# Performance work log

Measured on AMD Instinct MI355X. Metric: run time of the kernel, lower is better.

Reference implementation:

```python
import jax, jax.numpy as jnp
import numpy as np

B, Q, M, H, D = 2, 2048, 2048, 16, 64
HID = H * D           # hidden_size == num_heads * head_size
K_LEN = M + Q         # key/value length after memory concat
EPS = 1e-3            # keras LayerNormalization default epsilon
RAMP = 32             # Adaptive_Span ramp_size
NEG = -1e9


def setup_inputs() -> dict:
    key = jax.random.key(0)
    ks = jax.random.split(key, 12)
    s = 0.02
    return {
        "query": jax.random.normal(ks[0], (B, Q, HID), jnp.float32),
        "memory": jax.random.normal(ks[1], (B, M, HID), jnp.float32),
        "Wq": jax.random.normal(ks[2], (HID, H * D), jnp.float32) * s,
        "Wk": jax.random.normal(ks[3], (HID, H * D), jnp.float32) * s,
        "Wv": jax.random.normal(ks[4], (HID, H * D), jnp.float32) * s,
        "Wo": jax.random.normal(ks[5], (H * D, HID), jnp.float32) * s,
        "Wr": jax.random.normal(ks[6], (HID, H * D), jnp.float32) * s,
        "gamma_mem": jnp.ones((HID,), jnp.float32),
        "beta_mem": jnp.zeros((HID,), jnp.float32),
        "gamma_q": jnp.ones((HID,), jnp.float32),
        "beta_q": jnp.zeros((HID,), jnp.float32),
        "r_w_bias": jax.random.normal(ks[7], (1, H, 1, D), jnp.float32) * s,
        "r_r_bias": jax.random.normal(ks[8], (1, H, 1, D), jnp.float32) * s,
        "span_val": jnp.zeros((1, H, 1, 1), jnp.float32),
    }


def _layer_norm(x, gamma, beta):
    mu = jnp.mean(x, axis=-1, keepdims=True)
    var = jnp.mean(jnp.square(x - mu), axis=-1, keepdims=True)
    return (x - mu) * jax.lax.rsqrt(var + EPS) * gamma + beta


def _rel_shift(x):
    # Transformer-XL relative shift on [B,H,Q,K]
    b, h, q, k = x.shape
    x = jnp.pad(x, ((0, 0), (0, 0), (0, 0), (1, 0)))
    x = x.reshape(b, h, k + 1, q)[:, :, 1:, :]
    return x.reshape(b, h, q, k)


def reference(query, memory, Wq, Wk, Wv, Wo, Wr,
              gamma_mem, beta_mem, gamma_q, beta_q,
              r_w_bias, r_r_bias, span_val):
    kv = jnp.concatenate([memory, query], axis=1)          # [B,K,HID]
    kv = _layer_norm(kv, gamma_mem, beta_mem)
    q_in = _layer_norm(query, gamma_q, beta_q)

    # sinusoidal relative position embedding, positions K-1 .. 0
    pos_seq = jnp.arange(K_LEN - 1, -1, -1, dtype=jnp.float32)
    inv_freq = 1.0 / (10000.0 ** (jnp.arange(0, HID, 2, dtype=jnp.float32) / HID))
    sin_inp = pos_seq[:, None] * inv_freq[None, :]
    pos_emb = jnp.concatenate([jnp.sin(sin_inp), jnp.cos(sin_inp)], axis=-1)  # [K,HID]

    q = (q_in @ Wq).reshape(B, Q, H, D).transpose(0, 2, 1, 3)      # [B,H,Q,D]
    k = (kv @ Wk).reshape(B, K_LEN, H, D).transpose(0, 2, 1, 3)    # [B,H,K,D]
    v = (kv @ Wv).reshape(B, K_LEN, H, D).transpose(0, 2, 1, 3)    # [B,H,K,D]
    rel = (pos_emb @ Wr).reshape(K_LEN, H, D).transpose(1, 0, 2)   # [H,K,D]

    AD = jnp.einsum('bhqd,bhkd->bhqk', q + r_w_bias, k)
    BD = _rel_shift(jnp.einsum('bhqd,hkd->bhqk', q + r_r_bias, rel))
    logits = (AD + BD) / D                                          # note: /head_size, not sqrt

    # causal bias over the query block, zeros over memory columns
    causal = jnp.triu(jnp.ones((Q, Q), jnp.float32), 1) * NEG
    bias = jnp.concatenate([jnp.zeros((Q, M), jnp.float32), causal], axis=-1)
    logits = logits + bias[None, None]

    w = jax.nn.softmax(logits, axis=-1)                             # [B,H,Q,K]

    # adaptive span masking (static current_val path)
    mt = jnp.arange(Q, dtype=jnp.float32)
    span_mask = jnp.clip((mt[None, None, None, :] + span_val * Q) / (RAMP + 1), 0.0, 1.0)
    full_mask = jnp.concatenate(
        [jnp.ones((1, H, 1, M), jnp.float32),
         jnp.broadcast_to(span_mask, (1, H, 1, Q))], axis=-1)       # [1,H,1,K]
    w = w * full_mask
    w = w / (jnp.sum(w, axis=-1, keepdims=True) + 1e-8)

    out = jnp.einsum('bhqk,bhkd->bhqd', w, v)
    out = out.transpose(0, 2, 1, 3).reshape(B, Q, H * D)
    return out @ Wo
```

## Files before the change

kernel.cpp:

```cpp
#include <hip/hip_runtime.h>
#include <hip/hip_bf16.h>
#include <math.h>

#define B_   2
#define Q_   2048
#define M_   2048
#define H_   16
#define D_   64
#define HID_ 1024
#define KL_  4096
#define RT_  128
#define WT_  64
#define LSCL 0.022542110013890053f

typedef short short8 __attribute__((ext_vector_type(8)));
typedef short short4v __attribute__((ext_vector_type(4)));
typedef float f32x4 __attribute__((ext_vector_type(4)));
typedef float f32x16 __attribute__((ext_vector_type(16)));
typedef unsigned int uint2v __attribute__((ext_vector_type(2)));

__device__ __forceinline__ void async_copy16(const void* g, void* l) {
  __builtin_amdgcn_global_load_lds((const __attribute__((address_space(1))) unsigned int*)g,
                                   (__attribute__((address_space(3))) unsigned int*)l,
                                   16, 0, 0);
}

__device__ __forceinline__ float ldin(const void* p, size_t i, int md) {
  return md ? ((const float*)p)[i] : __bfloat162float(((const __hip_bfloat16*)p)[i]);
}

__device__ __forceinline__ short bfbits(float v) {
  __hip_bfloat16 t = __float2bfloat16(v);
  return *(short*)&t;
}

__device__ __forceinline__ float fexp2(float x) { return exp2f(x); }

__global__ __launch_bounds__(256) void detect_kernel(const unsigned int* __restrict__ q,
                                                     int* __restrict__ flag) {
  __shared__ int cnt;
  if (threadIdx.x == 0) cnt = 0;
  __syncthreads();
  int ins = 0;
#pragma unroll
  for (int i = 0; i < 4; i++) {
    unsigned int u = q[threadIdx.x * 4 + i];
    int e0 = (int)((u >> 7) & 0xffu);
    int e1 = (int)((u >> 23) & 0xffu);
    if (e0 == 0xff || e0 < 102 || e0 > 140) ins++;
    if (e1 == 0xff || e1 < 102 || e1 > 140) ins++;
  }
  atomicAdd(&cnt, ins);
  __syncthreads();
  if (threadIdx.x == 0) *flag = (cnt > 512) ? 1 : 0;
}

__global__ __launch_bounds__(256) void wtpe_kernel(
    const void* __restrict__ s0, const void* __restrict__ s1, const void* __restrict__ s2,
    const void* __restrict__ s3, const void* __restrict__ s4,
    __hip_bfloat16* __restrict__ d0, __hip_bfloat16* __restrict__ d1,
    __hip_bfloat16* __restrict__ d2, __hip_bfloat16* __restrict__ d3,
    __hip_bfloat16* __restrict__ d4, __hip_bfloat16* __restrict__ pe,
    const int* __restrict__ mode) {
  const int tid = threadIdx.x;
  if (blockIdx.z >= 5) {
    const int p = (blockIdx.z - 5) * 256 + blockIdx.y * 16 + blockIdx.x;
    const float pos = (float)(KL_ - 1 - p);
#pragma unroll
    for (int i = 0; i < 4; i++) {
      int c = tid * 4 + i;
      int f = (c < 512) ? c : c - 512;
      float invf = fexp2(-(float)f * (13.287712379549449f / 512.0f));
      float a = pos * invf;
      float v = (c < 512) ? __sinf(a) : __cosf(a);
      pe[(size_t)p * HID_ + c] = __float2bfloat16(v);
    }
    return;
  }
  const int md = *mode;
  const void* src; __hip_bfloat16* dst;
  switch (blockIdx.z) {
    case 0: src = s0; dst = d0; break;
    case 1: src = s1; dst = d1; break;
    case 2: src = s2; dst = d2; break;
    case 3: src = s3; dst = d3; break;
    default: src = s4; dst = d4; break;
  }
  const int r0 = blockIdx.x * 64, c0 = blockIdx.y * 64;
  __shared__ __hip_bfloat16 t[64][65];
  const int col = tid & 63, r4 = tid >> 6;
#pragma unroll
  for (int i = 0; i < 16; i++)
    t[r4 + i * 4][col] = __float2bfloat16(ldin(src, (size_t)(r0 + r4 + i * 4) * HID_ + c0 + col, md));
  __syncthreads();
#pragma unroll
  for (int i = 0; i < 16; i++)
    dst[(size_t)(c0 + r4 + i * 4) * HID_ + r0 + col] = t[col][r4 + i * 4];
}

__global__ __launch_bounds__(256) void ln_kernel(
    const void* __restrict__ mem, const void* __restrict__ qry,
    const void* __restrict__ gmem, const void* __restrict__ bmem,
    const void* __restrict__ gq, const void* __restrict__ bq,
    __hip_bfloat16* __restrict__ kvout, __hip_bfloat16* __restrict__ qout,
    const int* __restrict__ mode) {
  const int md = *mode;
  const int row = blockIdx.x;
  const void* src;
  const void* gamma; const void* beta;
  size_t base;
  __hip_bfloat16* dst;
  if (row < B_ * KL_) {
    const int b = row / KL_, j = row % KL_;
    if (j < M_) { src = mem; base = ((size_t)b * M_ + j) * HID_; }
    else        { src = qry; base = ((size_t)b * Q_ + (j - M_)) * HID_; }
    gamma = gmem; beta = bmem;
    dst = kvout + (size_t)row * HID_;
  } else {
    const int r = row - B_ * KL_;
    src = qry; base = (size_t)r * HID_;
    gamma = gq; beta = bq;
    dst = qout + (size_t)r * HID_;
  }
  const int tid = threadIdx.x;
  float x[4];
  float s = 0.f, ss = 0.f;
#pragma unroll
  for (int i = 0; i < 4; i++) {
    x[i] = ldin(src, base + i * 256 + tid, md);
    s += x[i]; ss += x[i] * x[i];
  }
#pragma unroll
  for (int o = 32; o > 0; o >>= 1) { s += __shfl_down(s, o); ss += __shfl_down(ss, o); }
  __shared__ float red[8];
  if ((tid & 63) == 0) { red[(tid >> 6) * 2] = s; red[(tid >> 6) * 2 + 1] = ss; }
  __syncthreads();
  float ts = 0.f, tss = 0.f;
#pragma unroll
  for (int i = 0; i < 4; i++) { ts += red[i * 2]; tss += red[i * 2 + 1]; }
  const float mu = ts * (1.f / 1024.f);
  const float var = tss * (1.f / 1024.f) - mu * mu;
  const float rs = rsqrtf(var + 1e-3f);
#pragma unroll
  for (int i = 0; i < 4; i++) {
    int c = i * 256 + tid;
    dst[c] = __float2bfloat16((x[i] - mu) * rs * ldin(gamma, c, md) + ldin(beta, c, md));
  }
}

template <int WRITE_MODE_SWITCH>
__device__ __forceinline__ void gemm_body(const __hip_bfloat16* __restrict__ A,
                                          const __hip_bfloat16* __restrict__ BT,
                                          void* __restrict__ C, int md, float scl) {
  __shared__ __attribute__((aligned(16))) __hip_bfloat16 sA[128 * 32];
  __shared__ __attribute__((aligned(16))) __hip_bfloat16 sB[128 * 32];
  const int tid = threadIdx.x;
  const int lane = tid & 63;
  const int w = tid >> 6;
  const int quad = lane >> 4, l16 = lane & 15;
  const int m0 = blockIdx.x * 128;
  const int n0 = blockIdx.y * 128;
  const int wm = (w >> 1) * 64, wn = (w & 1) * 64;
  const f32x4 fz = {0.f, 0.f, 0.f, 0.f};

  f32x4 acc[4][4];
#pragma unroll
  for (int i = 0; i < 4; i++)
#pragma unroll
    for (int j = 0; j < 4; j++) acc[i][j] = fz;

  for (int kk = 0; kk < HID_ / 32; kk++) {
    const int k0 = kk * 32;
    __syncthreads();
#pragma unroll
    for (int t = 0; t < 2; t++) {
      int c = (w * 2 + t) * 64 + lane;
      int row = c >> 2;
      int cid = (c & 3) ^ (row & 3);
      async_copy16(A + (size_t)(m0 + row) * HID_ + k0 + cid * 8, (char*)sA + c * 16);
      async_copy16(BT + (size_t)(n0 + row) * HID_ + k0 + cid * 8, (char*)sB + c * 16);
    }
    __syncthreads();
    short8 af[4], bf[4];
#pragma unroll
    for (int mt = 0; mt < 4; mt++) {
      int r = wm + mt * 16 + l16;
      af[mt] = *(const short8*)((const char*)sA + r * 64 + ((quad ^ (r & 3)) * 16));
    }
#pragma unroll
    for (int nt = 0; nt < 4; nt++) {
      int r = wn + nt * 16 + l16;
      bf[nt] = *(const short8*)((const char*)sB + r * 64 + ((quad ^ (r & 3)) * 16));
    }
#pragma unroll
    for (int mt = 0; mt < 4; mt++)
#pragma unroll
      for (int nt = 0; nt < 4; nt++)
        acc[mt][nt] = __builtin_amdgcn_mfma_f32_16x16x32_bf16(af[mt], bf[nt], acc[mt][nt], 0, 0, 0);
  }
#pragma unroll
  for (int mt = 0; mt < 4; mt++)
#pragma unroll
    for (int nt = 0; nt < 4; nt++)
#pragma unroll
      for (int rg = 0; rg < 4; rg++) {
        int r = m0 + wm + mt * 16 + quad * 4 + rg;
        int cc = n0 + wn + nt * 16 + l16;
        size_t idx = (size_t)r * HID_ + cc;
        if (WRITE_MODE_SWITCH && md) ((float*)C)[idx] = acc[mt][nt][rg];
        else ((__hip_bfloat16*)C)[idx] = __float2bfloat16(acc[mt][nt][rg] * scl);
      }
}

__global__ __launch_bounds__(256) void gemm_bt128(const __hip_bfloat16* __restrict__ A,
                                                  const __hip_bfloat16* __restrict__ BT,
                                                  __hip_bfloat16* __restrict__ C, float scl) {
  gemm_body<0>(A, BT, (void*)C, 0, scl);
}

__global__ __launch_bounds__(256) void gemm_out(const __hip_bfloat16* __restrict__ A,
                                                const __hip_bfloat16* __restrict__ BT,
                                                void* __restrict__ C,
                                                const int* __restrict__ mode) {
  gemm_body<1>(A, BT, C, *mode, 1.0f);
}

__global__ __launch_bounds__(256) void gemm_q(const __hip_bfloat16* __restrict__ A,
                                              const __hip_bfloat16* __restrict__ BT,
                                              const void* __restrict__ rwb,
                                              const void* __restrict__ rrb,
                                              __hip_bfloat16* __restrict__ qw,
                                              __hip_bfloat16* __restrict__ qr,
                                              const int* __restrict__ mode) {
  const int md = *mode;
  __shared__ __attribute__((aligned(16))) __hip_bfloat16 sA[128 * 32];
  __shared__ __attribute__((aligned(16))) __hip_bfloat16 sB[128 * 32];
  const int tid = threadIdx.x;
  const int lane = tid & 63;
  const int w = tid >> 6;
  const int quad = lane >> 4, l16 = lane & 15;
  const int m0 = blockIdx.x * 128;
  const int n0 = blockIdx.y * 128;
  const int wm = (w >> 1) * 64, wn = (w & 1) * 64;
  const f32x4 fz = {0.f, 0.f, 0.f, 0.f};

  f32x4 acc[4][4];
#pragma unroll
  for (int i = 0; i < 4; i++)
#pragma unroll
    for (int j = 0; j < 4; j++) acc[i][j] = fz;

  for (int kk = 0; kk < HID_ / 32; kk++) {
    const int k0 = kk * 32;
    __syncthreads();
#pragma unroll
    for (int t = 0; t < 2; t++) {
      int c = (w * 2 + t) * 64 + lane;
      int row = c >> 2;
      int cid = (c & 3) ^ (row & 3);
      async_copy16(A + (size_t)(m0 + row) * HID_ + k0 + cid * 8, (char*)sA + c * 16);
      async_copy16(BT + (size_t)(n0 + row) * HID_ + k0 + cid * 8, (char*)sB + c * 16);
    }
    __syncthreads();
    short8 af[4], bf[4];
#pragma unroll
    for (int mt = 0; mt < 4; mt++) {
      int r = wm + mt * 16 + l16;
      af[mt] = *(const short8*)((const char*)sA + r * 64 + ((quad ^ (r & 3)) * 16));
    }
#pragma unroll
    for (int nt = 0; nt < 4; nt++) {
      int r = wn + nt * 16 + l16;
      bf[nt] = *(const short8*)((const char*)sB + r * 64 + ((quad ^ (r & 3)) * 16));
    }
#pragma unroll
    for (int mt = 0; mt < 4; mt++)
#pragma unroll
      for (int nt = 0; nt < 4; nt++)
        acc[mt][nt] = __builtin_amdgcn_mfma_f32_16x16x32_bf16(af[mt], bf[nt], acc[mt][nt], 0, 0, 0);
  }
  float bw[4], br[4];
#pragma unroll
  for (int nt = 0; nt < 4; nt++) {
    int cc = n0 + wn + nt * 16 + l16;
    bw[nt] = ldin(rwb, cc, md);
    br[nt] = ldin(rrb, cc, md);
  }
#pragma unroll
  for (int mt = 0; mt < 4; mt++)
#pragma unroll
    for (int nt = 0; nt < 4; nt++)
#pragma unroll
      for (int rg = 0; rg < 4; rg++) {
        int r = m0 + wm + mt * 16 + quad * 4 + rg;
        int cc = n0 + wn + nt * 16 + l16;
        size_t idx = (size_t)r * HID_ + cc;
        float a = acc[mt][nt][rg];
        qw[idx] = __float2bfloat16((a + bw[nt]) * LSCL);
        qr[idx] = __float2bfloat16((a + br[nt]) * LSCL);
      }
}

__global__ __launch_bounds__(256) void gemm_dualv(const __hip_bfloat16* __restrict__ A,
                                                  const __hip_bfloat16* __restrict__ BT,
                                                  __hip_bfloat16* __restrict__ C0,
                                                  __hip_bfloat16* __restrict__ vpt) {
  __shared__ __attribute__((aligned(16))) __hip_bfloat16 sA[128 * 32];
  __shared__ __attribute__((aligned(16))) __hip_bfloat16 sB[128 * 32];
  __shared__ __attribute__((aligned(16))) short sT[128 * 136];
  const int tid = threadIdx.x;
  const int lane = tid & 63;
  const int w = tid >> 6;
  const int quad = lane >> 4, l16 = lane & 15;
  const int m0 = blockIdx.x * 128;
  const int n0 = blockIdx.y * 128;
  const int wm = (w >> 1) * 64, wn = (w & 1) * 64;
  const f32x4 fz = {0.f, 0.f, 0.f, 0.f};

  f32x4 acc[4][4];
#pragma unroll
  for (int i = 0; i < 4; i++)
#pragma unroll
    for (int j = 0; j < 4; j++) acc[i][j] = fz;

  for (int kk = 0; kk < HID_ / 32; kk++) {
    const int k0 = kk * 32;
    __syncthreads();
#pragma unroll
    for (int t = 0; t < 2; t++) {
      int c = (w * 2 + t) * 64 + lane;
      int row = c >> 2;
      int cid = (c & 3) ^ (row & 3);
      async_copy16(A + (size_t)(m0 + row) * HID_ + k0 + cid * 8, (char*)sA + c * 16);
      async_copy16(BT + (size_t)(n0 + row) * HID_ + k0 + cid * 8, (char*)sB + c * 16);
    }
    __syncthreads();
    short8 af[4], bf[4];
#pragma unroll
    for (int mt = 0; mt < 4; mt++) {
      int r = wm + mt * 16 + l16;
      af[mt] = *(const short8*)((const char*)sA + r * 64 + ((quad ^ (r & 3)) * 16));
    }
#pragma unroll
    for (int nt = 0; nt < 4; nt++) {
      int r = wn + nt * 16 + l16;
      bf[nt] = *(const short8*)((const char*)sB + r * 64 + ((quad ^ (r & 3)) * 16));
    }
#pragma unroll
    for (int mt = 0; mt < 4; mt++)
#pragma unroll
      for (int nt = 0; nt < 4; nt++)
        acc[mt][nt] = __builtin_amdgcn_mfma_f32_16x16x32_bf16(af[mt], bf[nt], acc[mt][nt], 0, 0, 0);
  }
  if (n0 < HID_) {
#pragma unroll
    for (int mt = 0; mt < 4; mt++)
#pragma unroll
      for (int nt = 0; nt < 4; nt++)
#pragma unroll
        for (int rg = 0; rg < 4; rg++) {
          int r = m0 + wm + mt * 16 + quad * 4 + rg;
          int cc = n0 + wn + nt * 16 + l16;
          C0[(size_t)r * HID_ + cc] = __float2bfloat16(acc[mt][nt][rg]);
        }
  } else {
#pragma unroll
    for (int mt = 0; mt < 4; mt++)
#pragma unroll
      for (int nt = 0; nt < 4; nt++) {
        int r = wm + mt * 16 + quad * 4;
        int cc = wn + nt * 16 + l16;
        short4v pk;
#pragma unroll
        for (int rg = 0; rg < 4; rg++) pk[rg] = bfbits(acc[mt][nt][rg]);
        *(short4v*)&sT[cc * 136 + r] = pk;
      }
    __syncthreads();
    const int b = m0 >> 12;
    const int j0g = m0 & (KL_ - 1);
    const int cg0 = n0 - HID_;
#pragma unroll
    for (int it = 0; it < 16; it++) {
      int cc = it * 8 + w * 2 + (lane >> 5);
      int jj = (lane & 31) * 4;
      int cg = cg0 + cc;
      int h = cg >> 6, d = cg & 63;
      short4v v = *(const short4v*)&sT[cc * 136 + jj];
      *(short4v*)(vpt + (((size_t)(b * H_ + h)) * D_ + d) * KL_ + j0g + jj) = v;
    }
  }
}

__global__ __launch_bounds__(256, 2) void attn_kernel(
    const __hip_bfloat16* __restrict__ qpw, const __hip_bfloat16* __restrict__ qpr,
    const __hip_bfloat16* __restrict__ kp, const __hip_bfloat16* __restrict__ vpt,
    const __hip_bfloat16* __restrict__ relp,
    const void* __restrict__ spanv, __hip_bfloat16* __restrict__ attn_out,
    const int* __restrict__ mode) {
  const int md = *mode;
  const int bid = blockIdx.x;
  int rk = (bid >> 3) & 15;
  if (bid & 256) rk ^= 15;
  const int i0 = rk << 7;
  const int bh = (bid & 7) + 8 * (bid >> 7);
  const int b = bh >> 4, h = bh & 15;

  const int tid = threadIdx.x;
  const int lane = tid & 63;
  const int w = tid >> 6;
  const int l31 = lane & 31, hi = lane >> 5;
  const int di = w * 32 + l31;
  const int iRow = i0 + di;

  __shared__ __attribute__((aligned(16))) __hip_bfloat16 sk[64 * 64];
  __shared__ __attribute__((aligned(16))) __hip_bfloat16 srel[192 * 64];
  __shared__ __attribute__((aligned(16))) __hip_bfloat16 svt[64 * 64];
  __shared__ __attribute__((aligned(16))) short sTP[128 * 100];

  const int rb = di * 200;
  const int sw = l31 & 7;

  const __hip_bfloat16* kbase = kp + (size_t)b * KL_ * HID_ + h * D_;
  const __hip_bfloat16* vtb = vpt + ((size_t)(b * H_ + h)) * D_ * KL_;
  const float sv = ldin(spanv, h, md);
  const float svQ = sv * (float)Q_;
  const int pb0 = Q_ - RT_ - i0;
  const int wof = (3 - w) * 32;
  const int ntiles = ((M_ + i0 + RT_ - 1) >> 6) + 1;

  const f32x16 z16 = {0.f,0.f,0.f,0.f,0.f,0.f,0.f,0.f,0.f,0.f,0.f,0.f,0.f,0.f,0.f,0.f};

  short8 qf[4], qrf[4];
  {
    const size_t qofs = ((size_t)(b * Q_ + iRow)) * HID_ + h * D_;
#pragma unroll
    for (int ks = 0; ks < 4; ks++) {
      qf[ks]  = *(const short8*)(qpw + qofs + ks * 16 + hi * 8);
      qrf[ks] = *(const short8*)(qpr + qofs + ks * 16 + hi * 8);
    }
  }

  {
#pragma unroll
    for (int t = 0; t < 2; t++) {
      int c = (w * 2 + t) * 64 + lane;
      int row = c >> 3;
      int cid = (c & 7) ^ (row & 7);
      async_copy16(kbase + (size_t)row * HID_ + cid * 8, (char*)sk + c * 16);
      async_copy16(vtb + (size_t)row * KL_ + cid * 8, (char*)svt + c * 16);
    }
#pragma unroll
    for (int t = 0; t < 6; t++) {
      int c = (w * 6 + t) * 64 + lane;
      int row = c >> 3;
      int cid = (c & 7) ^ (row & 7);
      int p = pb0 + row; p = p < KL_ ? p : KL_ - 1;
      async_copy16(relp + (size_t)p * HID_ + h * D_ + cid * 8, (char*)srel + c * 16);
    }
  }

  float mrow = -3e38f, lrow = 0.f, dfrow = 0.f;
  f32x16 oacc[2];
  oacc[0] = z16; oacc[1] = z16;
  int rot = 0;

  for (int kt = 0; kt < ntiles; kt++) {
    const int j0 = kt * WT_;

    __syncthreads();

    short8 rK[2], rR[2], rV[2];
    const bool pf = (kt + 1 < ntiles);
    {
      int j0n = j0 + WT_; if (j0n > KL_ - WT_) j0n = KL_ - WT_;
#pragma unroll
      for (int t = 0; t < 2; t++) {
        int c = (w * 2 + t) * 64 + lane;
        int row = c >> 3;
        int cid = (c & 7) ^ (row & 7);
        rK[t] = *(const short8*)(kbase + (size_t)(j0n + row) * HID_ + cid * 8);
        rV[t] = *(const short8*)(vtb + (size_t)row * KL_ + j0n + cid * 8);
        int p = pb0 + (kt + 1) * 64 + 128 + row; p = p < KL_ ? p : KL_ - 1;
        rR[t] = *(const short8*)(relp + (size_t)p * HID_ + h * D_ + cid * 8);
      }
    }
    __builtin_amdgcn_sched_barrier(0);

    __builtin_amdgcn_s_setprio(1);
    f32x16 S[2];
    S[0] = z16; S[1] = z16;
#pragma unroll
    for (int mt = 0; mt < 2; mt++) {
      const char* rowp = (const char*)sk + (mt * 32 + l31) * 128;
#pragma unroll
      for (int ks = 0; ks < 4; ks++) {
        short8 af = *(const short8*)(rowp + (((ks * 2 + hi) ^ sw) * 16));
        S[mt] = __builtin_amdgcn_mfma_f32_32x32x16_bf16(af, qf[ks], S[mt], 0, 0, 0);
      }
    }

#pragma unroll
    for (int mt = 0; mt < 3; mt++) {
      f32x16 T = z16;
      int rr = wof + mt * 32 + l31 + rot; if (rr >= 192) rr -= 192;
      const char* rowp = (const char*)srel + rr * 128;
#pragma unroll
      for (int ks = 0; ks < 4; ks++) {
        short8 af = *(const short8*)(rowp + (((ks * 2 + hi) ^ sw) * 16));
        T = __builtin_amdgcn_mfma_f32_32x32x16_bf16(af, qrf[ks], T, 0, 0, 0);
      }
#pragma unroll
      for (int r2 = 0; r2 < 4; r2++) {
        short4v pk;
#pragma unroll
        for (int r4 = 0; r4 < 4; r4++) pk[r4] = bfbits(T[r2 * 4 + r4]);
        *(short4v*)((char*)sTP + rb + (mt * 32 + 8 * r2 + 4 * hi) * 2) = pk;
      }
    }
    __builtin_amdgcn_s_setprio(0);

    {
      const char* tb2 = (const char*)sTP + rb + (31 - l31 + 4 * hi) * 2;
#pragma unroll
      for (int mt = 0; mt < 2; mt++)
#pragma unroll
        for (int r2 = 0; r2 < 4; r2++)
#pragma unroll
          for (int r4 = 0; r4 < 4; r4++)
            S[mt][r2 * 4 + r4] +=
                __bfloat162float(*(const __hip_bfloat16*)(tb2 + (mt * 32 + 8 * r2 + r4) * 2));
    }

    const bool causalT = (j0 + WT_ - 1 - i0) > M_;
    float mnew = mrow;
#pragma unroll
    for (int mt = 0; mt < 2; mt++)
#pragma unroll
      for (int r2 = 0; r2 < 4; r2++)
#pragma unroll
        for (int r4 = 0; r4 < 4; r4++) {
          float v = S[mt][r2 * 4 + r4];
          if (causalT) {
            int j = j0 + mt * 32 + 8 * r2 + 4 * hi + r4;
            if (j - iRow > M_) v = -1e30f;
          }
          S[mt][r2 * 4 + r4] = v;
          mnew = fmaxf(mnew, v);
        }
    mnew = fmaxf(mnew, __shfl_xor(mnew, 32));
    if (!__all(mnew - mrow <= 8.f)) {
      const float alpha = fexp2(mrow - mnew);
      mrow = mnew;
      lrow *= alpha; dfrow *= alpha;
#pragma unroll
      for (int dt = 0; dt < 2; dt++)
#pragma unroll
        for (int rg = 0; rg < 16; rg++) oacc[dt][rg] *= alpha;
    }

    const bool maskT = (j0 + WT_ > M_) && ((float)j0 < (float)M_ + 33.f - svQ);
    short8 paf[4];
#pragma unroll
    for (int mt = 0; mt < 2; mt++) {
      unsigned Pp[4][2];
#pragma unroll
      for (int r2 = 0; r2 < 4; r2++) {
        short4v g;
#pragma unroll
        for (int r4 = 0; r4 < 4; r4++) {
          float pv = fexp2(S[mt][r2 * 4 + r4] - mrow);
          lrow += pv;
          float pm = pv;
          if (maskT) {
            int j = j0 + mt * 32 + 8 * r2 + 4 * hi + r4;
            if (j >= M_) {
              float t0 = (float)(j - M_) + svQ;
              float mk = fminf(fmaxf(t0 * (1.0f / 33.0f), 0.f), 1.f);
              pm = pv * mk;
              dfrow += pv - pm;
            }
          }
          g[r4] = bfbits(pm);
        }
        union { short4v s; unsigned u[2]; } cv; cv.s = g;
        Pp[r2][0] = cv.u[0]; Pp[r2][1] = cv.u[1];
      }
#pragma unroll
      for (int half = 0; half < 2; half++) {
        uint2v rA = __builtin_amdgcn_permlane32_swap(Pp[half * 2][0], Pp[half * 2 + 1][0], false, false);
        uint2v rB = __builtin_amdgcn_permlane32_swap(Pp[half * 2][1], Pp[half * 2 + 1][1], false, false);
        union { unsigned u[4]; short8 s; } asm8;
        asm8.u[0] = rA[0]; asm8.u[1] = rB[0]; asm8.u[2] = rA[1]; asm8.u[3] = rB[1];
        paf[mt * 2 + half] = asm8.s;
      }
    }

    __builtin_amdgcn_s_setprio(1);
#pragma unroll
    for (int dt = 0; dt < 2; dt++) {
      const char* rowp = (const char*)svt + (dt * 32 + l31) * 128;
#pragma unroll
      for (int ks = 0; ks < 4; ks++) {
        short8 bfv = *(const short8*)(rowp + (((ks * 2 + hi) ^ sw) * 16));
        oacc[dt] = __builtin_amdgcn_mfma_f32_32x32x16_bf16(bfv, paf[ks], oacc[dt], 0, 0, 0);
      }
    }
    __builtin_amdgcn_s_setprio(0);

    __syncthreads();

    if (pf) {
#pragma unroll
      for (int t = 0; t < 2; t++) {
        int c = (w * 2 + t) * 64 + lane;
        int row = c >> 3;
        *(short8*)((char*)sk + c * 16) = rK[t];
        *(short8*)((char*)svt + c * 16) = rV[t];
        *(short8*)((char*)srel + (rot + row) * 128 + (c & 7) * 16) = rR[t];
      }
    }
    rot += 64; if (rot == 192) rot = 0;
  }

  lrow += __shfl_xor(lrow, 32);
  dfrow += __shfl_xor(dfrow, 32);
  const float denom = (lrow - dfrow) + 1e-8f * lrow;
  const float rdenom = 1.f / denom;
  __hip_bfloat16* ob = attn_out + ((size_t)(b * Q_ + iRow)) * HID_ + h * D_;
#pragma unroll
  for (int dt = 0; dt < 2; dt++)
#pragma unroll
    for (int r2 = 0; r2 < 4; r2++) {
      short4v o;
#pragma unroll
      for (int r4 = 0; r4 < 4; r4++) o[r4] = bfbits(oacc[dt][r2 * 4 + r4] * rdenom);
      *(short4v*)(ob + dt * 32 + 8 * r2 + 4 * hi) = o;
    }
}

extern "C" void kernel_launch(void* const* d_in, const int* in_sizes, int n_in,
                              void* d_out, int out_size, void* d_ws, size_t ws_size,
                              hipStream_t stream) {
  const void* query  = d_in[0];
  const void* memory = d_in[1];
  const void* Wq = d_in[2];
  const void* Wk = d_in[3];
  const void* Wv = d_in[4];
  const void* Wo = d_in[5];
  const void* Wr = d_in[6];
  const void* gmem = d_in[7];
  const void* bmem = d_in[8];
  const void* gq = d_in[9];
  const void* bq = d_in[10];
  const void* rwb = d_in[11];
  const void* rrb = d_in[12];
  const void* spanv = d_in[13];

  char* ws = (char*)d_ws;
  size_t off = 0;
  auto alloc = [&](size_t bytes) -> char* {
    char* p = ws + off;
    off += (bytes + 255) & ~(size_t)255;
    return p;
  };
  int* flag = (int*)alloc(256);
  const size_t SZ_W = (size_t)HID_ * HID_ * 2;
  __hip_bfloat16* wqT = (__hip_bfloat16*)alloc(SZ_W);
  __hip_bfloat16* wkT = (__hip_bfloat16*)alloc(SZ_W);
  __hip_bfloat16* wvT = (__hip_bfloat16*)alloc(SZ_W);
  __hip_bfloat16* wrT = (__hip_bfloat16*)alloc(SZ_W);
  __hip_bfloat16* woT = (__hip_bfloat16*)alloc(SZ_W);
  __hip_bfloat16* kvln = (__hip_bfloat16*)alloc((size_t)B_ * KL_ * HID_ * 2);
  __hip_bfloat16* qln  = (__hip_bfloat16*)alloc((size_t)B_ * Q_ * HID_ * 2);
  __hip_bfloat16* pe   = (__hip_bfloat16*)alloc((size_t)KL_ * HID_ * 2);
  __hip_bfloat16* qpw  = (__hip_bfloat16*)alloc((size_t)B_ * Q_ * HID_ * 2);
  __hip_bfloat16* qpr  = (__hip_bfloat16*)alloc((size_t)B_ * Q_ * HID_ * 2);
  __hip_bfloat16* kpb  = (__hip_bfloat16*)alloc((size_t)B_ * KL_ * HID_ * 2);
  __hip_bfloat16* vptb = (__hip_bfloat16*)alloc((size_t)B_ * KL_ * HID_ * 2);
  __hip_bfloat16* relp = (__hip_bfloat16*)alloc((size_t)KL_ * HID_ * 2);
  __hip_bfloat16* aout = (__hip_bfloat16*)alloc((size_t)B_ * Q_ * HID_ * 2);

  dim3 tb(256);
  detect_kernel<<<dim3(1), tb, 0, stream>>>((const unsigned int*)query, flag);

  wtpe_kernel<<<dim3(16, 16, 21), tb, 0, stream>>>(Wq, Wk, Wv, Wr, Wo,
                                                   wqT, wkT, wvT, wrT, woT, pe, flag);

  ln_kernel<<<dim3(B_ * KL_ + B_ * Q_), tb, 0, stream>>>(memory, query, gmem, bmem, gq, bq,
                                                         kvln, qln, flag);

  gemm_q<<<dim3(B_ * Q_ / 128, HID_ / 128), tb, 0, stream>>>(qln, wqT, rwb, rrb, qpw, qpr, flag);
  gemm_dualv<<<dim3(B_ * KL_ / 128, 2 * HID_ / 128), tb, 0, stream>>>(kvln, wkT, kpb, vptb);
  gemm_bt128<<<dim3(KL_ / 128, HID_ / 128), tb, 0, stream>>>(pe, wrT, relp, 1.0f);

  attn_kernel<<<dim3((Q_ / RT_) * H_ * B_), tb, 0, stream>>>(qpw, qpr, kpb, vptb, relp, spanv, aout, flag);

  gemm_out<<<dim3(B_ * Q_ / 128, HID_ / 128), tb, 0, stream>>>(aout, woT, d_out, flag);

  (void)in_sizes; (void)n_in; (void)out_size; (void)ws_size;
}
```

Before: 497.0 us.

## Load V fragments directly to registers and double-buffer K/rel tiles to drop a barrier

V^T fragments for the PV MFMA are now loaded straight from global memory into registers, with a one-tile register prefetch (vA/vB), instead of being staged through shared memory. K tiles are double-buffered in LDS and the rel ring grows from 192 to 256 rows, so each iteration needs one __syncthreads instead of two. This is meant to cut LDS traffic and barrier stalls in the attention loop. The cost is 16 extra short8 registers per thread, which may lower occupancy, plus uncoalesced per-lane global V reads.

```diff
diff --git a/kernel.cpp b/kernel.cpp
--- a/kernel.cpp
+++ b/kernel.cpp
@@ -412,9 +412,8 @@
   const int di = w * 32 + l31;
   const int iRow = i0 + di;
 
-  __shared__ __attribute__((aligned(16))) __hip_bfloat16 sk[64 * 64];
-  __shared__ __attribute__((aligned(16))) __hip_bfloat16 srel[192 * 64];
-  __shared__ __attribute__((aligned(16))) __hip_bfloat16 svt[64 * 64];
+  __shared__ __attribute__((aligned(16))) __hip_bfloat16 sk[2 * 64 * 64];
+  __shared__ __attribute__((aligned(16))) __hip_bfloat16 srel[256 * 64];
   __shared__ __attribute__((aligned(16))) short sTP[128 * 100];
 
   const int rb = di * 200;
@@ -440,6 +439,13 @@
     }
   }
 
+  short8 vA[8], vB[8];
+#pragma unroll
+  for (int dt = 0; dt < 2; dt++)
+#pragma unroll
+    for (int ks = 0; ks < 4; ks++)
+      vA[dt * 4 + ks] = *(const short8*)(vtb + (size_t)(dt * 32 + l31) * KL_ + ks * 16 + hi * 8);
+
   {
 #pragma unroll
     for (int t = 0; t < 2; t++) {
@@ -447,7 +453,6 @@
       int row = c >> 3;
       int cid = (c & 7) ^ (row & 7);
       async_copy16(kbase + (size_t)row * HID_ + cid * 8, (char*)sk + c * 16);
-      async_copy16(vtb + (size_t)row * KL_ + cid * 8, (char*)svt + c * 16);
     }
 #pragma unroll
     for (int t = 0; t < 6; t++) {
@@ -464,25 +469,31 @@
   oacc[0] = z16; oacc[1] = z16;
   int rot = 0;
 
+  __syncthreads();
+
   for (int kt = 0; kt < ntiles; kt++) {
     const int j0 = kt * WT_;
-
-    __syncthreads();
-
-    short8 rK[2], rR[2], rV[2];
+    const char* skr = (const char*)sk + (kt & 1) * 8192;
+    char* skw = (char*)sk + ((kt + 1) & 1) * 8192;
     const bool pf = (kt + 1 < ntiles);
+    int j0n = j0 + WT_; if (j0n > KL_ - WT_) j0n = KL_ - WT_;
+
+    short8 rK[2], rR[2];
     {
-      int j0n = j0 + WT_; if (j0n > KL_ - WT_) j0n = KL_ - WT_;
 #pragma unroll
       for (int t = 0; t < 2; t++) {
         int c = (w * 2 + t) * 64 + lane;
         int row = c >> 3;
         int cid = (c & 7) ^ (row & 7);
         rK[t] = *(const short8*)(kbase + (size_t)(j0n + row) * HID_ + cid * 8);
-        rV[t] = *(const short8*)(vtb + (size_t)row * KL_ + j0n + cid * 8);
-        int p = pb0 + (kt + 1) * 64 + 128 + row; p = p < KL_ ? p : KL_ - 1;
+        int p = pb0 + kt * 64 + 192 + row; p = p < KL_ ? p : KL_ - 1;
         rR[t] = *(const short8*)(relp + (size_t)p * HID_ + h * D_ + cid * 8);
       }
+#pragma unroll
+      for (int dt = 0; dt < 2; dt++)
+#pragma unroll
+        for (int ks = 0; ks < 4; ks++)
+          vB[dt * 4 + ks] = *(const short8*)(vtb + (size_t)(dt * 32 + l31) * KL_ + j0n + ks * 16 + hi * 8);
     }
     __builtin_amdgcn_sched_barrier(0);
 
@@ -491,7 +502,7 @@
     S[0] = z16; S[1] = z16;
 #pragma unroll
     for (int mt = 0; mt < 2; mt++) {
-      const char* rowp = (const char*)sk + (mt * 32 + l31) * 128;
+      const char* rowp = skr + (mt * 32 + l31) * 128;
 #pragma unroll
       for (int ks = 0; ks < 4; ks++) {
         short8 af = *(const short8*)(rowp + (((ks * 2 + hi) ^ sw) * 16));
@@ -502,7 +513,7 @@
 #pragma unroll
     for (int mt = 0; mt < 3; mt++) {
       f32x16 T = z16;
-      int rr = wof + mt * 32 + l31 + rot; if (rr >= 192) rr -= 192;
+      int rr = (wof + mt * 32 + l31 + rot) & 255;
       const char* rowp = (const char*)srel + rr * 128;
 #pragma unroll
       for (int ks = 0; ks < 4; ks++) {
@@ -597,29 +608,27 @@
 
     __builtin_amdgcn_s_setprio(1);
 #pragma unroll
-    for (int dt = 0; dt < 2; dt++) {
-      const char* rowp = (const char*)svt + (dt * 32 + l31) * 128;
-#pragma unroll
-      for (int ks = 0; ks < 4; ks++) {
-        short8 bfv = *(const short8*)(rowp + (((ks * 2 + hi) ^ sw) * 16));
-        oacc[dt] = __builtin_amdgcn_mfma_f32_32x32x16_bf16(bfv, paf[ks], oacc[dt], 0, 0, 0);
-      }
-    }
+    for (int dt = 0; dt < 2; dt++)
+#pragma unroll
+      for (int ks = 0; ks < 4; ks++)
+        oacc[dt] = __builtin_amdgcn_mfma_f32_32x32x16_bf16(vA[dt * 4 + ks], paf[ks], oacc[dt], 0, 0, 0);
     __builtin_amdgcn_s_setprio(0);
-
-    __syncthreads();
 
     if (pf) {
 #pragma unroll
       for (int t = 0; t < 2; t++) {
         int c = (w * 2 + t) * 64 + lane;
         int row = c >> 3;
-        *(short8*)((char*)sk + c * 16) = rK[t];
-        *(short8*)((char*)svt + c * 16) = rV[t];
-        *(short8*)((char*)srel + (rot + row) * 128 + (c & 7) * 16) = rR[t];
-      }
-    }
-    rot += 64; if (rot == 192) rot = 0;
+        *(short8*)(skw + c * 16) = rK[t];
+        int cr = (rot + 192 + row) & 255;
+        *(short8*)((char*)srel + cr * 128 + (c & 7) * 16) = rR[t];
+      }
+    }
+#pragma unroll
+    for (int i = 0; i < 8; i++) vA[i] = vB[i];
+    rot = (rot + 64) & 255;
+
+    __syncthreads();
   }
 
   lrow += __shfl_xor(lrow, 32);
```

Measured after the change: 514.0 us. 1.03x slower.

## Double GEMM K-tile to 64 and tree-reduce attention row max and sum

Applied to the files above, without the earlier changes.

The projection GEMMs now stage 64-wide K slices in LDS with an 8-way XOR swizzle, halving the number of barrier-separated load phases per tile. gemm_dualv aliases its transpose buffer onto the A/B staging area to keep LDS use flat, which needs an extra barrier before the transpose write. In the attention kernel, the causal mask is applied in a separate pass, and the row max and row sum are computed as shallow trees instead of serial chains to shorten dependency latency. The larger tiles raise LDS per block and may lower occupancy.

```diff
diff --git a/kernel.cpp b/kernel.cpp
--- a/kernel.cpp
+++ b/kernel.cpp
@@ -152,8 +152,8 @@
 __device__ __forceinline__ void gemm_body(const __hip_bfloat16* __restrict__ A,
                                           const __hip_bfloat16* __restrict__ BT,
                                           void* __restrict__ C, int md, float scl) {
-  __shared__ __attribute__((aligned(16))) __hip_bfloat16 sA[128 * 32];
-  __shared__ __attribute__((aligned(16))) __hip_bfloat16 sB[128 * 32];
+  __shared__ __attribute__((aligned(16))) __hip_bfloat16 sA[128 * 64];
+  __shared__ __attribute__((aligned(16))) __hip_bfloat16 sB[128 * 64];
   const int tid = threadIdx.x;
   const int lane = tid & 63;
   const int w = tid >> 6;
@@ -169,34 +169,37 @@
 #pragma unroll
     for (int j = 0; j < 4; j++) acc[i][j] = fz;
 
-  for (int kk = 0; kk < HID_ / 32; kk++) {
-    const int k0 = kk * 32;
-    __syncthreads();
-#pragma unroll
-    for (int t = 0; t < 2; t++) {
-      int c = (w * 2 + t) * 64 + lane;
-      int row = c >> 2;
-      int cid = (c & 3) ^ (row & 3);
+  for (int kk = 0; kk < HID_ / 64; kk++) {
+    const int k0 = kk * 64;
+    __syncthreads();
+#pragma unroll
+    for (int t = 0; t < 4; t++) {
+      int c = (w * 4 + t) * 64 + lane;
+      int row = c >> 3;
+      int cid = (c & 7) ^ (row & 7);
       async_copy16(A + (size_t)(m0 + row) * HID_ + k0 + cid * 8, (char*)sA + c * 16);
       async_copy16(BT + (size_t)(n0 + row) * HID_ + k0 + cid * 8, (char*)sB + c * 16);
     }
     __syncthreads();
-    short8 af[4], bf[4];
-#pragma unroll
-    for (int mt = 0; mt < 4; mt++) {
-      int r = wm + mt * 16 + l16;
-      af[mt] = *(const short8*)((const char*)sA + r * 64 + ((quad ^ (r & 3)) * 16));
-    }
-#pragma unroll
-    for (int nt = 0; nt < 4; nt++) {
-      int r = wn + nt * 16 + l16;
-      bf[nt] = *(const short8*)((const char*)sB + r * 64 + ((quad ^ (r & 3)) * 16));
-    }
-#pragma unroll
-    for (int mt = 0; mt < 4; mt++)
-#pragma unroll
-      for (int nt = 0; nt < 4; nt++)
-        acc[mt][nt] = __builtin_amdgcn_mfma_f32_16x16x32_bf16(af[mt], bf[nt], acc[mt][nt], 0, 0, 0);
+#pragma unroll
+    for (int half = 0; half < 2; half++) {
+      short8 af[4], bf[4];
+#pragma unroll
+      for (int mt = 0; mt < 4; mt++) {
+        int r = wm + mt * 16 + l16;
+        af[mt] = *(const short8*)((const char*)sA + r * 128 + (((half * 4 + quad) ^ (r & 7)) * 16));
+      }
+#pragma unroll
+      for (int nt = 0; nt < 4; nt++) {
+        int r = wn + nt * 16 + l16;
+        bf[nt] = *(const short8*)((const char*)sB + r * 128 + (((half * 4 + quad) ^ (r & 7)) * 16));
+      }
+#pragma unroll
+      for (int mt = 0; mt < 4; mt++)
+#pragma unroll
+        for (int nt = 0; nt < 4; nt++)
+          acc[mt][nt] = __builtin_amdgcn_mfma_f32_16x16x32_bf16(af[mt], bf[nt], acc[mt][nt], 0, 0, 0);
+    }
   }
 #pragma unroll
   for (int mt = 0; mt < 4; mt++)
@@ -233,8 +236,8 @@
                                               __hip_bfloat16* __restrict__ qr,
                                               const int* __restrict__ mode) {
   const int md = *mode;
-  __shared__ __attribute__((aligned(16))) __hip_bfloat16 sA[128 * 32];
-  __shared__ __attribute__((aligned(16))) __hip_bfloat16 sB[128 * 32];
+  __shared__ __attribute__((aligned(16))) __hip_bfloat16 sA[128 * 64];
+  __shared__ __attribute__((aligned(16))) __hip_bfloat16 sB[128 * 64];
   const int tid = threadIdx.x;
   const int lane = tid & 63;
   const int w = tid >> 6;
@@ -250,34 +253,37 @@
 #pragma unroll
     for (int j = 0; j < 4; j++) acc[i][j] = fz;
 
-  for (int kk = 0; kk < HID_ / 32; kk++) {
-    const int k0 = kk * 32;
-    __syncthreads();
-#pragma unroll
-    for (int t = 0; t < 2; t++) {
-      int c = (w * 2 + t) * 64 + lane;
-      int row = c >> 2;
-      int cid = (c & 3) ^ (row & 3);
+  for (int kk = 0; kk < HID_ / 64; kk++) {
+    const int k0 = kk * 64;
+    __syncthreads();
+#pragma unroll
+    for (int t = 0; t < 4; t++) {
+      int c = (w * 4 + t) * 64 + lane;
+      int row = c >> 3;
+      int cid = (c & 7) ^ (row & 7);
       async_copy16(A + (size_t)(m0 + row) * HID_ + k0 + cid * 8, (char*)sA + c * 16);
       async_copy16(BT + (size_t)(n0 + row) * HID_ + k0 + cid * 8, (char*)sB + c * 16);
     }
     __syncthreads();
-    short8 af[4], bf[4];
-#pragma unroll
-    for (int mt = 0; mt < 4; mt++) {
-      int r = wm + mt * 16 + l16;
-      af[mt] = *(const short8*)((const char*)sA + r * 64 + ((quad ^ (r & 3)) * 16));
-    }
-#pragma unroll
-    for (int nt = 0; nt < 4; nt++) {
-      int r = wn + nt * 16 + l16;
-      bf[nt] = *(const short8*)((const char*)sB + r * 64 + ((quad ^ (r & 3)) * 16));
-    }
-#pragma unroll
-    for (int mt = 0; mt < 4; mt++)
-#pragma unroll
-      for (int nt = 0; nt < 4; nt++)
-        acc[mt][nt] = __builtin_amdgcn_mfma_f32_16x16x32_bf16(af[mt], bf[nt], acc[mt][nt], 0, 0, 0);
+#pragma unroll
+    for (int half = 0; half < 2; half++) {
+      short8 af[4], bf[4];
+#pragma unroll
+      for (int mt = 0; mt < 4; mt++) {
+        int r = wm + mt * 16 + l16;
+        af[mt] = *(const short8*)((const char*)sA + r * 128 + (((half * 4 + quad) ^ (r & 7)) * 16));
+      }
+#pragma unroll
+      for (int nt = 0; nt < 4; nt++) {
+        int r = wn + nt * 16 + l16;
+        bf[nt] = *(const short8*)((const char*)sB + r * 128 + (((half * 4 + quad) ^ (r & 7)) * 16));
+      }
+#pragma unroll
+      for (int mt = 0; mt < 4; mt++)
+#pragma unroll
+        for (int nt = 0; nt < 4; nt++)
+          acc[mt][nt] = __builtin_amdgcn_mfma_f32_16x16x32_bf16(af[mt], bf[nt], acc[mt][nt], 0, 0, 0);
+    }
   }
   float bw[4], br[4];
 #pragma unroll
@@ -305,9 +311,10 @@
                                                   const __hip_bfloat16* __restrict__ BT,
                                                   __hip_bfloat16* __restrict__ C0,
                                                   __hip_bfloat16* __restrict__ vpt) {
-  __shared__ __attribute__((aligned(16))) __hip_bfloat16 sA[128 * 32];
-  __shared__ __attribute__((aligned(16))) __hip_bfloat16 sB[128 * 32];
-  __shared__ __attribute__((aligned(16))) short sT[128 * 136];
+  __shared__ __attribute__((aligned(16))) char smem[128 * 136 * 2];
+  __hip_bfloat16* sA = (__hip_bfloat16*)smem;
+  __hip_bfloat16* sB = (__hip_bfloat16*)(smem + 16384);
+  short* sT = (short*)smem;
   const int tid = threadIdx.x;
   const int lane = tid & 63;
   const int w = tid >> 6;
@@ -323,34 +330,37 @@
 #pragma unroll
     for (int j = 0; j < 4; j++) acc[i][j] = fz;
 
-  for (int kk = 0; kk < HID_ / 32; kk++) {
-    const int k0 = kk * 32;
-    __syncthreads();
-#pragma unroll
-    for (int t = 0; t < 2; t++) {
-      int c = (w * 2 + t) * 64 + lane;
-      int row = c >> 2;
-      int cid = (c & 3) ^ (row & 3);
+  for (int kk = 0; kk < HID_ / 64; kk++) {
+    const int k0 = kk * 64;
+    __syncthreads();
+#pragma unroll
+    for (int t = 0; t < 4; t++) {
+      int c = (w * 4 + t) * 64 + lane;
+      int row = c >> 3;
+      int cid = (c & 7) ^ (row & 7);
       async_copy16(A + (size_t)(m0 + row) * HID_ + k0 + cid * 8, (char*)sA + c * 16);
       async_copy16(BT + (size_t)(n0 + row) * HID_ + k0 + cid * 8, (char*)sB + c * 16);
     }
     __syncthreads();
-    short8 af[4], bf[4];
-#pragma unroll
-    for (int mt = 0; mt < 4; mt++) {
-      int r = wm + mt * 16 + l16;
-      af[mt] = *(const short8*)((const char*)sA + r * 64 + ((quad ^ (r & 3)) * 16));
-    }
-#pragma unroll
-    for (int nt = 0; nt < 4; nt++) {
-      int r = wn + nt * 16 + l16;
-      bf[nt] = *(const short8*)((const char*)sB + r * 64 + ((quad ^ (r & 3)) * 16));
-    }
-#pragma unroll
-    for (int mt = 0; mt < 4; mt++)
-#pragma unroll
-      for (int nt = 0; nt < 4; nt++)
-        acc[mt][nt] = __builtin_amdgcn_mfma_f32_16x16x32_bf16(af[mt], bf[nt], acc[mt][nt], 0, 0, 0);
+#pragma unroll
+    for (int half = 0; half < 2; half++) {
+      short8 af[4], bf[4];
+#pragma unroll
+      for (int mt = 0; mt < 4; mt++) {
+        int r = wm + mt * 16 + l16;
+        af[mt] = *(const short8*)((const char*)sA + r * 128 + (((half * 4 + quad) ^ (r & 7)) * 16));
+      }
+#pragma unroll
+      for (int nt = 0; nt < 4; nt++) {
+        int r = wn + nt * 16 + l16;
+        bf[nt] = *(const short8*)((const char*)sB + r * 128 + (((half * 4 + quad) ^ (r & 7)) * 16));
+      }
+#pragma unroll
+      for (int mt = 0; mt < 4; mt++)
+#pragma unroll
+        for (int nt = 0; nt < 4; nt++)
+          acc[mt][nt] = __builtin_amdgcn_mfma_f32_16x16x32_bf16(af[mt], bf[nt], acc[mt][nt], 0, 0, 0);
+    }
   }
   if (n0 < HID_) {
 #pragma unroll
@@ -364,6 +374,7 @@
           C0[(size_t)r * HID_ + cc] = __float2bfloat16(acc[mt][nt][rg]);
         }
   } else {
+    __syncthreads();
 #pragma unroll
     for (int mt = 0; mt < 4; mt++)
 #pragma unroll
@@ -532,21 +543,27 @@
     }
 
     const bool causalT = (j0 + WT_ - 1 - i0) > M_;
-    float mnew = mrow;
-#pragma unroll
-    for (int mt = 0; mt < 2; mt++)
-#pragma unroll
-      for (int r2 = 0; r2 < 4; r2++)
-#pragma unroll
-        for (int r4 = 0; r4 < 4; r4++) {
-          float v = S[mt][r2 * 4 + r4];
-          if (causalT) {
+    if (causalT) {
+#pragma unroll
+      for (int mt = 0; mt < 2; mt++)
+#pragma unroll
+        for (int r2 = 0; r2 < 4; r2++)
+#pragma unroll
+          for (int r4 = 0; r4 < 4; r4++) {
             int j = j0 + mt * 32 + 8 * r2 + 4 * hi + r4;
-            if (j - iRow > M_) v = -1e30f;
+            if (j - iRow > M_) S[mt][r2 * 4 + r4] = -1e30f;
           }
-          S[mt][r2 * 4 + r4] = v;
-          mnew = fmaxf(mnew, v);
-        }
+    }
+    float m8[8];
+#pragma unroll
+    for (int g = 0; g < 8; g++) {
+      int mt = g >> 2, r2 = g & 3;
+      m8[g] = fmaxf(fmaxf(S[mt][r2 * 4 + 0], S[mt][r2 * 4 + 1]),
+                    fmaxf(S[mt][r2 * 4 + 2], S[mt][r2 * 4 + 3]));
+    }
+    float mnew = fmaxf(mrow,
+        fmaxf(fmaxf(fmaxf(m8[0], m8[1]), fmaxf(m8[2], m8[3])),
+              fmaxf(fmaxf(m8[4], m8[5]), fmaxf(m8[6], m8[7]))));
     mnew = fmaxf(mnew, __shfl_xor(mnew, 32));
     if (!__all(mnew - mrow <= 8.f)) {
       const float alpha = fexp2(mrow - mnew);
@@ -566,10 +583,11 @@
 #pragma unroll
       for (int r2 = 0; r2 < 4; r2++) {
         short4v g;
+        float pvv[4];
 #pragma unroll
         for (int r4 = 0; r4 < 4; r4++) {
           float pv = fexp2(S[mt][r2 * 4 + r4] - mrow);
-          lrow += pv;
+          pvv[r4] = pv;
           float pm = pv;
           if (maskT) {
             int j = j0 + mt * 32 + 8 * r2 + 4 * hi + r4;
@@ -582,6 +600,7 @@
           }
           g[r4] = bfbits(pm);
         }
+        lrow += (pvv[0] + pvv[1]) + (pvv[2] + pvv[3]);
         union { short4v s; unsigned u[2]; } cv; cv.s = g;
         Pp[r2][0] = cv.u[0]; Pp[r2][1] = cv.u[1];
       }
```

Measured after the change: 476.1 us. -4.2%, faster.
